# Performance work log

Hardware: AMD Instinct MI355X
Metric: run time of the kernel (lower is better)

Reference implementation:

```python
import jax, jax.numpy as jnp
import numpy as np

COMMITMENT_WEIGHT = 0.25


def setup_inputs() -> dict:
    key = jax.random.key(0)
    k1, k2, k3, k4 = jax.random.split(key, 4)
    B, T, D, K, H = 8, 2048, 1024, 8192, 512
    features = jax.random.normal(k1, (B, T, D), dtype=jnp.float32)
    codebook = jax.random.normal(k2, (K, D), dtype=jnp.float32)
    w1 = jax.random.normal(k3, (D, H), dtype=jnp.float32) * (1.0 / np.sqrt(D))
    b1 = jnp.zeros((H,), dtype=jnp.float32)
    w2 = jax.random.normal(k4, (H, D), dtype=jnp.float32) * (1.0 / np.sqrt(H))
    b2 = jnp.zeros((D,), dtype=jnp.float32)
    return {"features": features, "codebook": codebook, "w1": w1, "b1": b1, "w2": w2, "b2": b2}


def reference(features, codebook, w1, b1, w2, b2):
    # --- nearest-codebook search (euclidean). |x|^2 term is constant per row,
    scores = -2.0 * jnp.einsum("btd,kd->btk", features, codebook) + jnp.sum(codebook * codebook, axis=-1)
    indices = jnp.argmin(scores, axis=-1)            # [B, T] int
    q = codebook[indices]                            # [B, T, D] gather

    # commitment loss: mse(sg(q), x) * weight
    diff = features - jax.lax.stop_gradient(q)
    loss = COMMITMENT_WEIGHT * jnp.mean(diff * diff)

    # straight-through estimator
    quantized = features + jax.lax.stop_gradient(q - features)

    # decoder MLP: Linear -> ReLU -> Linear
    h = jax.nn.relu(jnp.einsum("btd,dh->bth", quantized, w1) + b1)
    recon = jnp.einsum("bth,hd->btd", h, w2) + b2
    return recon, indices, loss
```

## Files before the change

### kernel.cpp

```cpp
#include <hip/hip_runtime.h>
#include <hip/hip_fp8.h>
#include <stdint.h>


#define MROWS  16384
#define DDIM   1024
#define KCODES 8192
#define HDIM   512
#define EROWS  16

typedef __attribute__((ext_vector_type(4))) float  f32x4;
typedef __attribute__((ext_vector_type(8))) __bf16 bf16x8;
typedef __attribute__((ext_vector_type(4))) int    i32x4;
typedef __attribute__((ext_vector_type(8))) int    i32x8;

__device__ __forceinline__ unsigned short f2bf(float f) {
  uint32_t b = __float_as_uint(f);
  b += 0x7FFFu + ((b >> 16) & 1u);
  return (unsigned short)(b >> 16);
}

__device__ __forceinline__ uint32_t f2fp8(float f) {
  return (uint32_t)__hip_fp8_e4m3(f).__x;
}

__device__ __forceinline__ uint32_t packkey(float s, int idx) {
  uint32_t u = __float_as_uint(s);
  u = ((int)u < 0) ? ~u : (u | 0x80000000u);
  return (u & 0xFFFFE000u) | (uint32_t)idx;
}
__device__ __forceinline__ float unpackkey(uint32_t k) {
  uint32_t u = k & 0xFFFFE000u;
  u = (u & 0x80000000u) ? (u ^ 0x80000000u) : ~u;
  return __uint_as_float(u);
}

__device__ __forceinline__ void gload_lds16(const void* g, void* l) {
  __builtin_amdgcn_global_load_lds(
      (__attribute__((address_space(1))) void*)(uintptr_t)g,
      (__attribute__((address_space(3))) void*)(uint32_t)(uintptr_t)l,
      16, 0, 0);
}

__device__ __forceinline__ f32x4 mfma_mx(i32x8 a, i32x8 b, f32x4 c) {
  return __builtin_amdgcn_mfma_scale_f32_16x16x128_f8f6f4(
      a, b, c, 0, 0, 0, 0x7F7F7F7F, 0, 0x7F7F7F7F);
}

__device__ __forceinline__ float waveReduceSum(float v) {
#pragma unroll
  for (int off = 32; off > 0; off >>= 1) v += __shfl_xor(v, off, 64);
  return v;
}

__global__ __launch_bounds__(256) void prep_kernel(
    const float* __restrict__ features, const float* __restrict__ codebook,
    const float* __restrict__ w1, const float* __restrict__ w2,
    uint8_t* __restrict__ xq8, uint8_t* __restrict__ cq8,
    unsigned short* __restrict__ cbb, float* __restrict__ cn,
    unsigned short* __restrict__ w1t, unsigned short* __restrict__ w2t) {
  __shared__ float wsum[4];
  __shared__ float tile[32][33];
  const int bid = blockIdx.x, t = threadIdx.x;
  if (bid < 8192) {
    const int id = bid * 256 + t;
    const float4 v0 = ((const float4*)features)[id * 2];
    const float4 v1 = ((const float4*)features)[id * 2 + 1];
    uint2 u;
    u.x = f2fp8(v0.x) | (f2fp8(v0.y) << 8) | (f2fp8(v0.z) << 16) |
          (f2fp8(v0.w) << 24);
    u.y = f2fp8(v1.x) | (f2fp8(v1.y) << 8) | (f2fp8(v1.z) << 16) |
          (f2fp8(v1.w) << 24);
    ((uint2*)xq8)[id] = u;
  } else if (bid < 16384) {
    const int k = bid - 8192;
    const float4 v = ((const float4*)(codebook + (size_t)k * DDIM))[t];
    ushort4 u;
    u.x = f2bf(v.x); u.y = f2bf(v.y); u.z = f2bf(v.z); u.w = f2bf(v.w);
    ((ushort4*)(cbb + (size_t)k * DDIM))[t] = u;
    const uint32_t p8 = f2fp8(v.x) | (f2fp8(v.y) << 8) | (f2fp8(v.z) << 16) |
                        (f2fp8(v.w) << 24);
    ((uint32_t*)(cq8 + (size_t)k * DDIM))[t] = p8;
    float p = v.x * v.x + v.y * v.y + v.z * v.z + v.w * v.w;
    p = waveReduceSum(p);
    if ((t & 63) == 0) wsum[t >> 6] = p;
    __syncthreads();
    if (t == 0) cn[k] = wsum[0] + wsum[1] + wsum[2] + wsum[3];
  } else {
    const float* src;
    unsigned short* dst;
    int R, C, t32;
    if (bid < 16896) { src = w1; dst = w1t; R = 1024; C = 512;
                       t32 = bid - 16384; }
    else             { src = w2; dst = w2t; R = 512;  C = 1024;
                       t32 = bid - 16896; }
    const int nct = C / 32;
    const int tr0 = (t32 / nct) * 32, tc0 = (t32 % nct) * 32;
    const int rr = t >> 3, cc = (t & 7) * 4;
    const float4 v = *(const float4*)(src + (size_t)(tr0 + rr) * C + tc0 + cc);
    tile[rr][cc + 0] = v.x; tile[rr][cc + 1] = v.y;
    tile[rr][cc + 2] = v.z; tile[rr][cc + 3] = v.w;
    __syncthreads();
    ushort4 o;
    o.x = f2bf(tile[cc + 0][rr]); o.y = f2bf(tile[cc + 1][rr]);
    o.z = f2bf(tile[cc + 2][rr]); o.w = f2bf(tile[cc + 3][rr]);
    *(ushort4*)(dst + (size_t)(tc0 + rr) * R + tr0 + cc) = o;
  }
}

__global__ __launch_bounds__(256, 3) void coarse_kernel(
    const uint8_t* __restrict__ xq,
    const uint8_t* __restrict__ cq,
    const float* __restrict__ cn,
    uint32_t* __restrict__ cand2)
{
  __shared__ char smem[34816];

  const int tid = threadIdx.x;
  const int l = tid & 63, w = tid >> 6;
  const int lr = l & 15, lg = l >> 4;
  const int wm = w >> 1, wn = w & 1;

  const int bid = blockIdx.x;
  const int xcd = bid & 7;
  const int local = bid >> 3;
  const int chunk = local >> 5;
  const int wi = local & 31;
  const int mb = xcd * 16 + (chunk >> 3) * 4 + (wi >> 3);
  const int nb = (chunk & 7) * 8 + (wi & 7);
  const int r0 = mb * 128, c0 = nb * 128;

  const int scolb = ((tid & 7) * 16) ^ (((tid >> 3) & 7) << 4);
  const uint8_t* aSrc = xq + (size_t)(r0 + (tid >> 3)) * DDIM + scolb;
  const uint8_t* bSrc = cq + (size_t)(c0 + (tid >> 3)) * DDIM + scolb;
  const int dBase = tid * 16;

  const int sxor = (lr & 7) << 4;
  const int kLo = (lg * 32) ^ sxor;
  const int kHi = (lg * 32 + 16) ^ sxor;
  const int aRow = (wm * 64 + lr) * 128;
  const int bRow = 16384 + (wn * 64 + lr) * 128;

#define STAGE(KT)                                                             \
  {                                                                           \
    _Pragma("unroll")                                                         \
    for (int j = 0; j < 4; ++j)                                               \
      gload_lds16(aSrc + (size_t)j * 32 * DDIM + (KT) * 128,                  \
                  smem + dBase + j * 4096);                                   \
    _Pragma("unroll")                                                         \
    for (int j = 0; j < 4; ++j)                                               \
      gload_lds16(bSrc + (size_t)j * 32 * DDIM + (KT) * 128,                  \
                  smem + 16384 + dBase + j * 4096);                           \
  }

#define LDFRAG(dst, off)                                                      \
  {                                                                           \
    i32x4 _lo = *(const i32x4*)(smem + (off) + kLo);                          \
    i32x4 _hi = *(const i32x4*)(smem + (off) + kHi);                          \
    dst = __builtin_shufflevector(_lo, _hi, 0, 1, 2, 3, 4, 5, 6, 7);          \
  }

  f32x4 acc[4][4];
#pragma unroll
  for (int mi = 0; mi < 4; ++mi)
#pragma unroll
    for (int ni = 0; ni < 4; ++ni) acc[mi][ni] = 0.0f;

#pragma unroll 1
  for (int kt = 0; kt < 8; ++kt) {
    __builtin_amdgcn_sched_barrier(0);
    STAGE(kt)
    __builtin_amdgcn_sched_barrier(0);
    __syncthreads();

    i32x8 bf[4];
#pragma unroll
    for (int ni = 0; ni < 4; ++ni) LDFRAG(bf[ni], bRow + ni * 2048)
#pragma unroll
    for (int mi = 0; mi < 4; ++mi) {
      i32x8 af;
      LDFRAG(af, aRow + mi * 2048)
      __builtin_amdgcn_s_setprio(1);
#pragma unroll
      for (int ni = 0; ni < 4; ++ni)
        acc[mi][ni] = mfma_mx(af, bf[ni], acc[mi][ni]);
      __builtin_amdgcn_s_setprio(0);
    }

    __builtin_amdgcn_sched_barrier(0);
    __syncthreads();
  }

  uint2* mrg = (uint2*)smem;
  const int slot = wn * 16 + lr;

  float cnv[4];
#pragma unroll
  for (int ni = 0; ni < 4; ++ni) cnv[ni] = cn[c0 + wn * 64 + ni * 16 + lr];

#pragma unroll
  for (int mi = 0; mi < 4; ++mi) {
#pragma unroll
    for (int r = 0; r < 4; ++r) {
      uint32_t k1 = 0xFFFFFFFFu, k2 = 0xFFFFFFFFu;
#pragma unroll
      for (int ni = 0; ni < 4; ++ni) {
        const float s = fmaf(-2.0f, acc[mi][ni][r], cnv[ni]);
        const uint32_t k = packkey(s, c0 + wn * 64 + ni * 16 + lr);
        if (k < k1) { k2 = k1; k1 = k; } else if (k < k2) { k2 = k; }
      }
      const int row = wm * 64 + mi * 16 + lg * 4 + r;
      uint2 e; e.x = k1; e.y = k2;
      mrg[row * 34 + slot] = e;
    }
  }
  __syncthreads();

  {
    const int row = tid >> 1, h = tid & 1;
    const uint4* mp = (const uint4*)(mrg + row * 34 + h * 16);
    uint32_t k1 = 0xFFFFFFFFu, k2 = 0xFFFFFFFFu;
#pragma unroll
    for (int j = 0; j < 8; ++j) {
      const uint4 v = mp[j];
      uint32_t a = (k1 < v.x) ? k1 : v.x;
      uint32_t b0 = (k1 < v.x) ? v.x : k1;
      uint32_t c = (k2 < v.y) ? k2 : v.y;
      k1 = a; k2 = (b0 < c) ? b0 : c;
      a = (k1 < v.z) ? k1 : v.z;
      b0 = (k1 < v.z) ? v.z : k1;
      c = (k2 < v.w) ? k2 : v.w;
      k1 = a; k2 = (b0 < c) ? b0 : c;
    }
    const uint32_t o1 = (uint32_t)__shfl_xor((int)k1, 1, 64);
    const uint32_t o2 = (uint32_t)__shfl_xor((int)k2, 1, 64);
    const uint32_t m1 = (k1 < o1) ? k1 : o1;
    const uint32_t hi = (k1 < o1) ? o1 : k1;
    const uint32_t lo2 = (k2 < o2) ? k2 : o2;
    const uint32_t m2 = (hi < lo2) ? hi : lo2;
    if (h == 0) {
      uint2 o; o.x = m1; o.y = m2;
      *((uint2*)(cand2 + ((size_t)(r0 + row) * 64 + nb) * 2)) = o;
    }
  }
#undef STAGE
#undef LDFRAG
}

__global__ __launch_bounds__(256) void rescore_kernel(
    const float* __restrict__ x, const float* __restrict__ cb,
    const uint32_t* __restrict__ cand2, int* __restrict__ idx_ws,
    float* __restrict__ out) {
  const int row = blockIdx.x * 4 + (threadIdx.x >> 6);
  const int l = threadIdx.x & 63;

  const uint2 pr = ((const uint2*)cand2)[(size_t)row * 64 + l];
  const uint32_t k1 = pr.x, k2 = pr.y;

  uint32_t bs = k1;
#pragma unroll
  for (int off = 1; off < 64; off <<= 1) {
    const uint32_t ob = (uint32_t)__shfl_xor((int)bs, off, 64);
    bs = (ob < bs) ? ob : bs;
  }
  const float smin = unpackkey(bs);
  const uint32_t thrkey = packkey(smin + 36.0f, 8191);
  unsigned long long mA = __ballot(k1 <= thrkey);
  unsigned long long mB = __ballot(k2 <= thrkey);

  if (__popcll(mA) + __popcll(mB) == 1) {
    if (l == 0) {
      const int code = (int)(bs & 8191u);
      idx_ws[row] = code;
      out[(size_t)MROWS * DDIM + row] = (float)code;
    }
    return;
  }

  const float4* x4 = (const float4*)(x + (size_t)row * DDIM);
  float4 xv[4];
#pragma unroll
  for (int i = 0; i < 4; ++i) xv[i] = x4[i * 64 + l];

  float bestS = __builtin_inff(); int bestI = KCODES;
#pragma unroll 1
  for (int half = 0; half < 2; ++half) {
    unsigned long long m = half ? mB : mA;
    const uint32_t myk = half ? k2 : k1;
    while (m) {
      const int b = __builtin_ctzll(m);
      m &= m - 1;
      const int code = __shfl((int)myk, b, 64) & 8191;
      const float4* c4 = (const float4*)(cb + (size_t)code * DDIM);
      float dot = 0.f, nn = 0.f;
#pragma unroll
      for (int i = 0; i < 4; ++i) {
        const float4 cv = c4[i * 64 + l];
        dot = fmaf(xv[i].x, cv.x, dot); dot = fmaf(xv[i].y, cv.y, dot);
        dot = fmaf(xv[i].z, cv.z, dot); dot = fmaf(xv[i].w, cv.w, dot);
        nn  = fmaf(cv.x, cv.x, nn);     nn  = fmaf(cv.y, cv.y, nn);
        nn  = fmaf(cv.z, cv.z, nn);     nn  = fmaf(cv.w, cv.w, nn);
      }
#pragma unroll
      for (int off = 32; off > 0; off >>= 1) {
        dot += __shfl_xor(dot, off, 64);
        nn  += __shfl_xor(nn,  off, 64);
      }
      const float sc = nn - 2.0f * dot;
      if (sc < bestS || (sc == bestS && code < bestI)) { bestS = sc; bestI = code; }
    }
  }
  if (l == 0) {
    idx_ws[row] = bestI;
    out[(size_t)MROWS * DDIM + row] = (float)bestI;
  }
}

template <int EPI>
__global__ __launch_bounds__(256) void gemm_bt_kernel(
    const unsigned short* __restrict__ A, const unsigned short* __restrict__ B,
    const float* __restrict__ bias, void* __restrict__ outp,
    int Nsize, int Kred, int nblk) {
  __shared__ unsigned short As[128 * 32];
  __shared__ unsigned short Bs[128 * 32];
  const int tid = threadIdx.x;
  const int l = tid & 63, w = tid >> 6;
  const int lr = l & 15, lg = l >> 4;
  const int wm = w >> 1, wn = w & 1;
  const int mb = blockIdx.x / nblk, nb = blockIdx.x % nblk;
  const int r0 = mb * 128, c0 = nb * 128;
  const int prow = tid >> 2, pcol = (tid & 3) * 8;

  f32x4 acc[4][4];
#pragma unroll
  for (int mi = 0; mi < 4; ++mi)
#pragma unroll
    for (int ni = 0; ni < 4; ++ni) acc[mi][ni] = 0.0f;

  const size_t aoff0 = (size_t)(r0 + prow) * Kred + pcol;
  const size_t aoff1 = aoff0 + (size_t)64 * Kred;
  const size_t boff0 = (size_t)(c0 + prow) * Kred + pcol;
  const size_t boff1 = boff0 + (size_t)64 * Kred;

  const int nks = Kred >> 5;
  for (int ks = 0; ks < nks; ++ks) {
    const int k0 = ks * 32;
    gload_lds16(A + aoff0 + k0, &As[tid * 8]);
    gload_lds16(A + aoff1 + k0, &As[2048 + tid * 8]);
    gload_lds16(B + boff0 + k0, &Bs[tid * 8]);
    gload_lds16(B + boff1 + k0, &Bs[2048 + tid * 8]);
    __syncthreads();

    bf16x8 af[4], bfv[4];
#pragma unroll
    for (int mi = 0; mi < 4; ++mi)
      af[mi] = *reinterpret_cast<const bf16x8*>(
          &As[(wm * 64 + mi * 16 + lr) * 32 + lg * 8]);
#pragma unroll
    for (int ni = 0; ni < 4; ++ni)
      bfv[ni] = *reinterpret_cast<const bf16x8*>(
          &Bs[(wn * 64 + ni * 16 + lr) * 32 + lg * 8]);
#pragma unroll
    for (int mi = 0; mi < 4; ++mi)
#pragma unroll
      for (int ni = 0; ni < 4; ++ni)
        acc[mi][ni] = __builtin_amdgcn_mfma_f32_16x16x32_bf16(
            af[mi], bfv[ni], acc[mi][ni], 0, 0, 0);
    __syncthreads();
  }

#pragma unroll
  for (int ni = 0; ni < 4; ++ni) {
    const int col = c0 + wn * 64 + ni * 16 + lr;
    const float bv = bias[col];
#pragma unroll
    for (int mi = 0; mi < 4; ++mi) {
#pragma unroll
      for (int r = 0; r < 4; ++r) {
        const int row = r0 + wm * 64 + mi * 16 + lg * 4 + r;
        const float v = acc[mi][ni][r] + bv;
        if (EPI == 1) {
          ((unsigned short*)outp)[(size_t)row * Nsize + col] =
              f2bf(fmaxf(v, 0.0f));
        } else {
          ((float*)outp)[(size_t)row * Nsize + col] = v;
        }
      }
    }
  }
}

__global__ __launch_bounds__(256) void epilogue_kernel(
    const float* __restrict__ x, const float* __restrict__ cb,
    const float* __restrict__ dec, const int* __restrict__ idx_ws,
    float* __restrict__ out, float* __restrict__ partial) {
  __shared__ float wsum[4];
  const int t = threadIdx.x;
  const int base = blockIdx.x * EROWS;

  int code[EROWS];
#pragma unroll
  for (int rr = 0; rr < EROWS; ++rr) code[rr] = idx_ws[base + rr];

  float lsum = 0.0f;
#pragma unroll
  for (int rr = 0; rr < EROWS; ++rr) {
    const int r = base + rr;
    const float4 dv = ((const float4*)(dec + (size_t)code[rr] * DDIM))[t];
    ((float4*)(out + (size_t)r * DDIM))[t] = dv;
    const float4 xv = ((const float4*)(x + (size_t)r * DDIM))[t];
    const float4 cv = ((const float4*)(cb + (size_t)code[rr] * DDIM))[t];
    const float ex = xv.x - cv.x, ey = xv.y - cv.y;
    const float ez = xv.z - cv.z, ew = xv.w - cv.w;
    lsum += ex * ex + ey * ey + ez * ez + ew * ew;
  }
  lsum = waveReduceSum(lsum);
  if ((t & 63) == 0) wsum[t >> 6] = lsum;
  __syncthreads();
  if (t == 0)
    partial[blockIdx.x] = wsum[0] + wsum[1] + wsum[2] + wsum[3];
}

__global__ __launch_bounds__(256) void loss_reduce_kernel(
    const float* __restrict__ partial, float* __restrict__ out) {
  __shared__ float wsum[4];
  const int t = threadIdx.x;
  float s = 0.0f;
#pragma unroll
  for (int j = 0; j < 4; ++j) s += partial[t * 4 + j];
  s = waveReduceSum(s);
  if ((t & 63) == 0) wsum[t >> 6] = s;
  __syncthreads();
  if (t == 0) {
    const float total = wsum[0] + wsum[1] + wsum[2] + wsum[3];
    out[(size_t)MROWS * DDIM + MROWS] = total * (0.25f / 16777216.0f);
  }
}

extern "C" void kernel_launch(void* const* d_in, const int* in_sizes, int n_in,
                              void* d_out, int out_size, void* d_ws,
                              size_t ws_size, hipStream_t stream) {
  const float* features = (const float*)d_in[0];
  const float* codebook = (const float*)d_in[1];
  const float* w1 = (const float*)d_in[2];
  const float* b1 = (const float*)d_in[3];
  const float* w2 = (const float*)d_in[4];
  const float* b2 = (const float*)d_in[5];
  float* out = (float*)d_out;
  char* ws = (char*)d_ws;

  uint8_t*        xq8 = (uint8_t*)(ws + 0);
  uint8_t*        cq8 = (uint8_t*)(ws + 16777216);
  unsigned short* cbb = (unsigned short*)(ws + 25165824);
  float*          cn  = (float*)(ws + 41943040);
  unsigned short* w1t = (unsigned short*)(ws + 41975808);
  unsigned short* w2t = (unsigned short*)(ws + 43024384);
  unsigned short* hb  = (unsigned short*)(ws + 44072960);
  float*          dec = (float*)(ws + 52461568);
  int*            idxw = (int*)(ws + 86016000);
  float*          lpart = (float*)(ws + 86081536);
  uint32_t*       cand2 = (uint32_t*)(ws + 52461568);

  prep_kernel<<<17408, 256, 0, stream>>>(features, codebook, w1, w2,
                                         xq8, cq8, cbb, cn, w1t, w2t);

  coarse_kernel<<<(MROWS / 128) * (KCODES / 128), 256, 0, stream>>>(
      xq8, cq8, cn, cand2);
  rescore_kernel<<<MROWS / 4, 256, 0, stream>>>(features, codebook, cand2,
                                                idxw, out);

  gemm_bt_kernel<1><<<64 * (HDIM / 128), 256, 0, stream>>>(
      cbb, w1t, b1, hb, HDIM, DDIM, HDIM / 128);
  gemm_bt_kernel<2><<<64 * (DDIM / 128), 256, 0, stream>>>(
      hb, w2t, b2, dec, DDIM, HDIM, DDIM / 128);

  epilogue_kernel<<<MROWS / EROWS, 256, 0, stream>>>(features, codebook, dec,
                                                     idxw, out, lpart);
  loss_reduce_kernel<<<1, 256, 0, stream>>>(lpart, out);
}
```

Before: 307.4 us.

## Fuse rescore into epilogue and load A fragments directly from global

```diff
diff --git a/kernel.cpp b/kernel.cpp
--- a/kernel.cpp
+++ b/kernel.cpp
@@ -7,7 +7,6 @@
 #define DDIM   1024
 #define KCODES 8192
 #define HDIM   512
-#define EROWS  16
 
 typedef __attribute__((ext_vector_type(4))) float  f32x4;
 typedef __attribute__((ext_vector_type(8))) __bf16 bf16x8;
@@ -131,35 +130,38 @@
   const int r0 = mb * 128, c0 = nb * 128;
 
   const int scolb = ((tid & 7) * 16) ^ (((tid >> 3) & 7) << 4);
-  const uint8_t* aSrc = xq + (size_t)(r0 + (tid >> 3)) * DDIM + scolb;
   const uint8_t* bSrc = cq + (size_t)(c0 + (tid >> 3)) * DDIM + scolb;
   const int dBase = tid * 16;
 
   const int sxor = (lr & 7) << 4;
   const int kLo = (lg * 32) ^ sxor;
   const int kHi = (lg * 32 + 16) ^ sxor;
-  const int aRow = (wm * 64 + lr) * 128;
-  const int bRow = 16384 + (wn * 64 + lr) * 128;
-
-#define STAGE(KT)                                                             \
+  const int bRow = (wn * 64 + lr) * 128;
+
+  const uint8_t* aG = xq + (size_t)(r0 + wm * 64 + lr) * DDIM + lg * 32;
+
+#define STAGE_B(KT)                                                           \
   {                                                                           \
     _Pragma("unroll")                                                         \
     for (int j = 0; j < 4; ++j)                                               \
-      gload_lds16(aSrc + (size_t)j * 32 * DDIM + (KT) * 128,                  \
+      gload_lds16(bSrc + (size_t)j * 32 * DDIM + (KT) * 128,                  \
                   smem + dBase + j * 4096);                                   \
-    _Pragma("unroll")                                                         \
-    for (int j = 0; j < 4; ++j)                                               \
-      gload_lds16(bSrc + (size_t)j * 32 * DDIM + (KT) * 128,                  \
-                  smem + 16384 + dBase + j * 4096);                           \
-  }
-
-#define LDFRAG(dst, off)                                                      \
+  }
+
+#define LDB(dst, off)                                                         \
   {                                                                           \
     i32x4 _lo = *(const i32x4*)(smem + (off) + kLo);                          \
     i32x4 _hi = *(const i32x4*)(smem + (off) + kHi);                          \
     dst = __builtin_shufflevector(_lo, _hi, 0, 1, 2, 3, 4, 5, 6, 7);          \
   }
 
+#define LDAG(dst, ptr)                                                        \
+  {                                                                           \
+    i32x4 _lo = *(const i32x4*)(ptr);                                         \
+    i32x4 _hi = *(const i32x4*)((ptr) + 16);                                  \
+    dst = __builtin_shufflevector(_lo, _hi, 0, 1, 2, 3, 4, 5, 6, 7);          \
+  }
+
   f32x4 acc[4][4];
 #pragma unroll
   for (int mi = 0; mi < 4; ++mi)
@@ -168,24 +170,24 @@
 
 #pragma unroll 1
   for (int kt = 0; kt < 8; ++kt) {
+    i32x8 af[4], bf[4];
     __builtin_amdgcn_sched_barrier(0);
-    STAGE(kt)
+    STAGE_B(kt)
+#pragma unroll
+    for (int mi = 0; mi < 4; ++mi)
+      LDAG(af[mi], aG + kt * 128 + (size_t)mi * 16 * DDIM)
     __builtin_amdgcn_sched_barrier(0);
     __syncthreads();
 
-    i32x8 bf[4];
-#pragma unroll
-    for (int ni = 0; ni < 4; ++ni) LDFRAG(bf[ni], bRow + ni * 2048)
-#pragma unroll
-    for (int mi = 0; mi < 4; ++mi) {
-      i32x8 af;
-      LDFRAG(af, aRow + mi * 2048)
-      __builtin_amdgcn_s_setprio(1);
+#pragma unroll
+    for (int ni = 0; ni < 4; ++ni) LDB(bf[ni], bRow + ni * 2048)
+    __builtin_amdgcn_s_setprio(1);
+#pragma unroll
+    for (int mi = 0; mi < 4; ++mi)
 #pragma unroll
       for (int ni = 0; ni < 4; ++ni)
-        acc[mi][ni] = mfma_mx(af, bf[ni], acc[mi][ni]);
-      __builtin_amdgcn_s_setprio(0);
-    }
+        acc[mi][ni] = mfma_mx(af[mi], bf[ni], acc[mi][ni]);
+    __builtin_amdgcn_s_setprio(0);
 
     __builtin_amdgcn_sched_barrier(0);
     __syncthreads();
@@ -243,77 +245,9 @@
       *((uint2*)(cand2 + ((size_t)(r0 + row) * 64 + nb) * 2)) = o;
     }
   }
-#undef STAGE
-#undef LDFRAG
-}
-
-__global__ __launch_bounds__(256) void rescore_kernel(
-    const float* __restrict__ x, const float* __restrict__ cb,
-    const uint32_t* __restrict__ cand2, int* __restrict__ idx_ws,
-    float* __restrict__ out) {
-  const int row = blockIdx.x * 4 + (threadIdx.x >> 6);
-  const int l = threadIdx.x & 63;
-
-  const uint2 pr = ((const uint2*)cand2)[(size_t)row * 64 + l];
-  const uint32_t k1 = pr.x, k2 = pr.y;
-
-  uint32_t bs = k1;
-#pragma unroll
-  for (int off = 1; off < 64; off <<= 1) {
-    const uint32_t ob = (uint32_t)__shfl_xor((int)bs, off, 64);
-    bs = (ob < bs) ? ob : bs;
-  }
-  const float smin = unpackkey(bs);
-  const uint32_t thrkey = packkey(smin + 36.0f, 8191);
-  unsigned long long mA = __ballot(k1 <= thrkey);
-  unsigned long long mB = __ballot(k2 <= thrkey);
-
-  if (__popcll(mA) + __popcll(mB) == 1) {
-    if (l == 0) {
-      const int code = (int)(bs & 8191u);
-      idx_ws[row] = code;
-      out[(size_t)MROWS * DDIM + row] = (float)code;
-    }
-    return;
-  }
-
-  const float4* x4 = (const float4*)(x + (size_t)row * DDIM);
-  float4 xv[4];
-#pragma unroll
-  for (int i = 0; i < 4; ++i) xv[i] = x4[i * 64 + l];
-
-  float bestS = __builtin_inff(); int bestI = KCODES;
-#pragma unroll 1
-  for (int half = 0; half < 2; ++half) {
-    unsigned long long m = half ? mB : mA;
-    const uint32_t myk = half ? k2 : k1;
-    while (m) {
-      const int b = __builtin_ctzll(m);
-      m &= m - 1;
-      const int code = __shfl((int)myk, b, 64) & 8191;
-      const float4* c4 = (const float4*)(cb + (size_t)code * DDIM);
-      float dot = 0.f, nn = 0.f;
-#pragma unroll
-      for (int i = 0; i < 4; ++i) {
-        const float4 cv = c4[i * 64 + l];
-        dot = fmaf(xv[i].x, cv.x, dot); dot = fmaf(xv[i].y, cv.y, dot);
-        dot = fmaf(xv[i].z, cv.z, dot); dot = fmaf(xv[i].w, cv.w, dot);
-        nn  = fmaf(cv.x, cv.x, nn);     nn  = fmaf(cv.y, cv.y, nn);
-        nn  = fmaf(cv.z, cv.z, nn);     nn  = fmaf(cv.w, cv.w, nn);
-      }
-#pragma unroll
-      for (int off = 32; off > 0; off >>= 1) {
-        dot += __shfl_xor(dot, off, 64);
-        nn  += __shfl_xor(nn,  off, 64);
-      }
-      const float sc = nn - 2.0f * dot;
-      if (sc < bestS || (sc == bestS && code < bestI)) { bestS = sc; bestI = code; }
-    }
-  }
-  if (l == 0) {
-    idx_ws[row] = bestI;
-    out[(size_t)MROWS * DDIM + row] = (float)bestI;
-  }
+#undef STAGE_B
+#undef LDB
+#undef LDAG
 }
 
 template <int EPI>
@@ -390,34 +324,89 @@
   }
 }
 
-__global__ __launch_bounds__(256) void epilogue_kernel(
+__global__ __launch_bounds__(256) void finish_kernel(
     const float* __restrict__ x, const float* __restrict__ cb,
-    const float* __restrict__ dec, const int* __restrict__ idx_ws,
+    const float* __restrict__ dec, const uint32_t* __restrict__ cand2,
     float* __restrict__ out, float* __restrict__ partial) {
   __shared__ float wsum[4];
-  const int t = threadIdx.x;
-  const int base = blockIdx.x * EROWS;
-
-  int code[EROWS];
-#pragma unroll
-  for (int rr = 0; rr < EROWS; ++rr) code[rr] = idx_ws[base + rr];
-
+  const int wid = threadIdx.x >> 6;
+  const int row = blockIdx.x * 4 + wid;
+  const int l = threadIdx.x & 63;
+
+  const uint2 pr = ((const uint2*)cand2)[(size_t)row * 64 + l];
+  const uint32_t k1 = pr.x, k2 = pr.y;
+
+  uint32_t bs = k1;
+#pragma unroll
+  for (int off = 1; off < 64; off <<= 1) {
+    const uint32_t ob = (uint32_t)__shfl_xor((int)bs, off, 64);
+    bs = (ob < bs) ? ob : bs;
+  }
+  const float smin = unpackkey(bs);
+  const uint32_t thrkey = packkey(smin + 36.0f, 8191);
+  unsigned long long mA = __ballot(k1 <= thrkey);
+  unsigned long long mB = __ballot(k2 <= thrkey);
+
+  int code;
+  if (__popcll(mA) + __popcll(mB) == 1) {
+    code = (int)(bs & 8191u);
+  } else {
+    const float4* x4 = (const float4*)(x + (size_t)row * DDIM);
+    float4 xv[4];
+#pragma unroll
+    for (int i = 0; i < 4; ++i) xv[i] = x4[i * 64 + l];
+    float bestS = __builtin_inff(); int bestI = KCODES;
+#pragma unroll 1
+    for (int half = 0; half < 2; ++half) {
+      unsigned long long m = half ? mB : mA;
+      const uint32_t myk = half ? k2 : k1;
+      while (m) {
+        const int b = __builtin_ctzll(m);
+        m &= m - 1;
+        const int cd = __shfl((int)myk, b, 64) & 8191;
+        const float4* c4 = (const float4*)(cb + (size_t)cd * DDIM);
+        float dot = 0.f, nn = 0.f;
+#pragma unroll
+        for (int i = 0; i < 4; ++i) {
+          const float4 cv = c4[i * 64 + l];
+          dot = fmaf(xv[i].x, cv.x, dot); dot = fmaf(xv[i].y, cv.y, dot);
+          dot = fmaf(xv[i].z, cv.z, dot); dot = fmaf(xv[i].w, cv.w, dot);
+          nn  = fmaf(cv.x, cv.x, nn);     nn  = fmaf(cv.y, cv.y, nn);
+          nn  = fmaf(cv.z, cv.z, nn);     nn  = fmaf(cv.w, cv.w, nn);
+        }
+#pragma unroll
+        for (int off = 32; off > 0; off >>= 1) {
+          dot += __shfl_xor(dot, off, 64);
+          nn  += __shfl_xor(nn,  off, 64);
+        }
+        const float sc = nn - 2.0f * dot;
+        if (sc < bestS || (sc == bestS && cd < bestI)) { bestS = sc; bestI = cd; }
+      }
+    }
+    code = bestI;
+  }
+
+  const float4* d4 = (const float4*)(dec + (size_t)code * DDIM);
+  const float4* x4 = (const float4*)(x + (size_t)row * DDIM);
+  const float4* c4 = (const float4*)(cb + (size_t)code * DDIM);
+  float4* o4 = (float4*)(out + (size_t)row * DDIM);
   float lsum = 0.0f;
 #pragma unroll
-  for (int rr = 0; rr < EROWS; ++rr) {
-    const int r = base + rr;
-    const float4 dv = ((const float4*)(dec + (size_t)code[rr] * DDIM))[t];
-    ((float4*)(out + (size_t)r * DDIM))[t] = dv;
-    const float4 xv = ((const float4*)(x + (size_t)r * DDIM))[t];
-    const float4 cv = ((const float4*)(cb + (size_t)code[rr] * DDIM))[t];
+  for (int i = 0; i < 4; ++i) {
+    const float4 dv = d4[i * 64 + l];
+    o4[i * 64 + l] = dv;
+    const float4 xv = x4[i * 64 + l];
+    const float4 cv = c4[i * 64 + l];
     const float ex = xv.x - cv.x, ey = xv.y - cv.y;
     const float ez = xv.z - cv.z, ew = xv.w - cv.w;
     lsum += ex * ex + ey * ey + ez * ez + ew * ew;
   }
+  if (l == 0) out[(size_t)MROWS * DDIM + row] = (float)code;
+
   lsum = waveReduceSum(lsum);
-  if ((t & 63) == 0) wsum[t >> 6] = lsum;
+  if (l == 0) wsum[wid] = lsum;
   __syncthreads();
-  if (t == 0)
+  if (threadIdx.x == 0)
     partial[blockIdx.x] = wsum[0] + wsum[1] + wsum[2] + wsum[3];
 }
 
@@ -427,7 +416,7 @@
   const int t = threadIdx.x;
   float s = 0.0f;
 #pragma unroll
-  for (int j = 0; j < 4; ++j) s += partial[t * 4 + j];
+  for (int j = 0; j < 16; ++j) s += partial[t * 16 + j];
   s = waveReduceSum(s);
   if ((t & 63) == 0) wsum[t >> 6] = s;
   __syncthreads();
@@ -457,24 +446,21 @@
   unsigned short* w2t = (unsigned short*)(ws + 43024384);
   unsigned short* hb  = (unsigned short*)(ws + 44072960);
   float*          dec = (float*)(ws + 52461568);
-  int*            idxw = (int*)(ws + 86016000);
-  float*          lpart = (float*)(ws + 86081536);
-  uint32_t*       cand2 = (uint32_t*)(ws + 52461568);
+  float*          lpart = (float*)(ws + 86016000);
+  uint32_t*       cand2 = (uint32_t*)(ws + 86032384);
 
   prep_kernel<<<17408, 256, 0, stream>>>(features, codebook, w1, w2,
                                          xq8, cq8, cbb, cn, w1t, w2t);
 
   coarse_kernel<<<(MROWS / 128) * (KCODES / 128), 256, 0, stream>>>(
       xq8, cq8, cn, cand2);
-  rescore_kernel<<<MROWS / 4, 256, 0, stream>>>(features, codebook, cand2,
-                                                idxw, out);
 
   gemm_bt_kernel<1><<<64 * (HDIM / 128), 256, 0, stream>>>(
       cbb, w1t, b1, hb, HDIM, DDIM, HDIM / 128);
   gemm_bt_kernel<2><<<64 * (DDIM / 128), 256, 0, stream>>>(
       hb, w2t, b2, dec, DDIM, HDIM, DDIM / 128);
 
-  epilogue_kernel<<<MROWS / EROWS, 256, 0, stream>>>(features, codebook, dec,
-                                                     idxw, out, lpart);
+  finish_kernel<<<MROWS / 4, 256, 0, stream>>>(features, codebook, dec,
+                                               cand2, out, lpart);
   loss_reduce_kernel<<<1, 256, 0, stream>>>(lpart, out);
 }
```

New measurement: 417.8 us. 35.9% more time.
